# Kernel optimization log

Hardware: AMD Instinct MI355X
Metric: run time of the kernel (lower is better)

Reference implementation:

```python
import jax, jax.numpy as jnp
import numpy as np
from jax import lax

NSAMPLE = 1024
SEM_NUM = 20


def weighted_fps(xyz, w, nsample):
    # xyz: [B,N,3], w: [B,N] -> idx [B,nsample] int32
    # Iterative weighted furthest point sampling: start at index 0, keep the
    # min squared distance to the selected set, pick argmax(min_dist * weight).
    B, N, _ = xyz.shape
    barange = jnp.arange(B)

    def step(carry, _):
        min_d, last = carry                      # [B,N], [B]
        lp = xyz[barange, last]                  # [B,3] last selected points
        d = jnp.sum((xyz - lp[:, None, :]) ** 2, axis=-1)  # [B,N]
        min_d = jnp.minimum(min_d, d)
        nxt = jnp.argmax(min_d * w, axis=1).astype(jnp.int32)
        return (min_d, nxt), nxt

    init = (jnp.full((B, N), 1e10, xyz.dtype), jnp.zeros((B,), jnp.int32))
    _, rest = lax.scan(step, init, None, length=nsample - 1)   # [nsample-1, B]
    idx = jnp.concatenate([jnp.zeros((1, B), jnp.int32), rest], axis=0)
    return idx.T                                               # [B, nsample]


def setup_inputs() -> dict:
    key = jax.random.key(0)
    k1, k2, k3 = jax.random.split(key, 3)
    B, N, C = 16, 16384, 128
    xyz = jax.random.normal(k1, (B, N, 3), dtype=jnp.float32)
    seg_feature = jax.random.normal(k2, (B, C, N), dtype=jnp.float32)
    seg_label = jax.random.randint(k3, (B, N), 0, SEM_NUM, dtype=jnp.int32)
    return {"xyz": xyz, "seg_feature": seg_feature, "seg_label": seg_label}


def reference(xyz, seg_feature, seg_label):
    # class frequency weights: count[b,c] = #points of class c in cloud b
    counts = jnp.sum(jax.nn.one_hot(seg_label, SEM_NUM, dtype=jnp.float32), axis=1)  # [B,SEM]
    seg_weights = jnp.take_along_axis(counts, seg_label, axis=1)                     # [B,N]
    idx = weighted_fps(lax.stop_gradient(xyz), seg_weights, NSAMPLE)                 # [B,S]
    sampled_xyz = jnp.take_along_axis(xyz, idx[:, :, None], axis=1)                  # [B,S,3]
    sample_seg_feature = jnp.take_along_axis(seg_feature, idx[:, None, :], axis=2)   # [B,C,S]
    sample_seg_label = jnp.take_along_axis(seg_label, idx, axis=1)                   # [B,S]
    return sampled_xyz, sample_seg_feature, sample_seg_label
```

## Files before the change

### kernel.cpp

```cpp
#include <hip/hip_runtime.h>


#define FPS_B   16
#define FPS_N   16384
#define FPS_C   128
#define FPS_S   1024
#define FPS_SEM 20
#define FPS_QB  4
#define FPS_MT  1024
#define FPS_MP  4

typedef unsigned long long ull;

__global__ void zero_slots(ull* part) {
  int i = blockIdx.x * blockDim.x + threadIdx.x;
  part[i] = 0ull;
}

__global__ __launch_bounds__(FPS_MT) void wfps_multi(
    const float* __restrict__ xyz,
    const int*   __restrict__ label,
    int*         __restrict__ idx_out,
    ull*         __restrict__ part)
{
  const int b = blockIdx.x & 15;
  const int q = blockIdx.x >> 4;
  const int t = threadIdx.x;

  __shared__ int counts[FPS_SEM];
  __shared__ ull wmax[FPS_S];

  if (t < FPS_SEM) counts[t] = 0;
  wmax[t] = 0ull;
  __syncthreads();

  const int* lab = label + b * FPS_N;
#pragma unroll
  for (int j = 0; j < 16; ++j)
    atomicAdd(&counts[lab[t + j * FPS_MT]], 1);
  __syncthreads();

  const float* xb = xyz + b * FPS_N * 3;
  float px[FPS_MP], py[FPS_MP], pz[FPS_MP], w[FPS_MP], mind[FPS_MP];
#pragma unroll
  for (int k = 0; k < FPS_MP; ++k) {
    int n = q * 4096 + k * 1024 + t;
    px[k] = xb[n * 3 + 0];
    py[k] = xb[n * 3 + 1];
    pz[k] = xb[n * 3 + 2];
    w[k] = (float)counts[lab[n]];
    mind[k] = 1e10f;
    asm("" : "+v"(px[k]), "+v"(py[k]), "+v"(pz[k]), "+v"(w[k]));
  }

  if (q == 0 && t == 0) idx_out[b * FPS_S] = 0;
  float lx = xb[0], ly = xb[1], lz = xb[2];

  ull* pb = part + b * (FPS_QB * FPS_S);

  for (int s = 1; s < FPS_S; ++s) {
    float bs = -1.0f;
    int bk = 0;
#pragma unroll
    for (int k = 0; k < FPS_MP; ++k) {
      float dx = __fsub_rn(px[k], lx);
      float dy = __fsub_rn(py[k], ly);
      float dz = __fsub_rn(pz[k], lz);
      float d  = __fadd_rn(__fadd_rn(__fmul_rn(dx, dx), __fmul_rn(dy, dy)),
                           __fmul_rn(dz, dz));
      float m = fminf(mind[k], d);
      mind[k] = m;
      float sc = __fmul_rn(m, w[k]);
      bool g = sc > bs;
      bs = g ? sc : bs;
      bk = g ? k : bk;
    }
    unsigned n = (unsigned)t + ((unsigned)bk << 10) + ((unsigned)q << 12);
    ull best = ((ull)__float_as_uint(bs) << 32) | (ull)(~n);

#pragma unroll
    for (int off = 32; off > 0; off >>= 1) {
      ull o = __shfl_xor(best, off, 64);
      best = (o > best) ? o : best;
    }
    if ((t & 63) == 0) atomicMax(&wmax[s], best);
    __syncthreads();

    if (t == 0) {
      ull loc = wmax[s];
      __hip_atomic_store(&pb[q * FPS_S + s], loc,
                         __ATOMIC_RELAXED, __HIP_MEMORY_SCOPE_AGENT);
      const int q1 = (q + 1) & 3, q2 = (q + 2) & 3, q3 = (q + 3) & 3;
      ull v1, v2, v3;
      do {
        v1 = __hip_atomic_load(&pb[q1 * FPS_S + s],
                               __ATOMIC_RELAXED, __HIP_MEMORY_SCOPE_AGENT);
        v2 = __hip_atomic_load(&pb[q2 * FPS_S + s],
                               __ATOMIC_RELAXED, __HIP_MEMORY_SCOPE_AGENT);
        v3 = __hip_atomic_load(&pb[q3 * FPS_S + s],
                               __ATOMIC_RELAXED, __HIP_MEMORY_SCOPE_AGENT);
      } while (!(v1 && v2 && v3));
      ull m = loc;
      m = (v1 > m) ? v1 : m;
      m = (v2 > m) ? v2 : m;
      m = (v3 > m) ? v3 : m;
      wmax[s] = m;
    }
    __syncthreads();

    ull g = wmax[s];
    int cur = (int)(~(unsigned)g);
    cur = __builtin_amdgcn_readfirstlane(cur);

    if (q == 0 && t == 0) idx_out[b * FPS_S + s] = cur;

    const float* qq = xb + 3 * cur;
    lx = qq[0]; ly = qq[1]; lz = qq[2];
  }
}

__global__ __launch_bounds__(1024)
__attribute__((amdgpu_waves_per_eu(4, 4)))
void wfps_single(
    const float* __restrict__ xyz,
    const int*   __restrict__ label,
    int*         __restrict__ idx_out)
{
  const int b = blockIdx.x;
  const int t = threadIdx.x;

  __shared__ int counts[FPS_SEM];
  __shared__ ull wmax[FPS_S];

  if (t < FPS_SEM) counts[t] = 0;
  wmax[t] = 0ull;
  __syncthreads();

  const int* lab = label + b * FPS_N;
  int mylab[16];
#pragma unroll
  for (int k = 0; k < 16; ++k) {
    mylab[k] = lab[t + k * 1024];
    atomicAdd(&counts[mylab[k]], 1);
  }
  __syncthreads();

  const float* xb = xyz + b * FPS_N * 3;
  float px[16], py[16], pz[16], w[16], mind[16];
#pragma unroll
  for (int k = 0; k < 16; ++k) {
    int n = t + k * 1024;
    px[k] = xb[n * 3 + 0];
    py[k] = xb[n * 3 + 1];
    pz[k] = xb[n * 3 + 2];
    w[k] = (float)counts[mylab[k]];
    mind[k] = 1e10f;
    asm("" : "+v"(px[k]), "+v"(py[k]), "+v"(pz[k]), "+v"(w[k]));
  }

  if (t == 0) idx_out[b * FPS_S] = 0;
  float lx = xb[0], ly = xb[1], lz = xb[2];

  for (int s = 1; s < FPS_S; ++s) {
    float bs = -1.0f;
    int bk = 0;
#pragma unroll
    for (int k = 0; k < 16; ++k) {
      float dx = __fsub_rn(px[k], lx);
      float dy = __fsub_rn(py[k], ly);
      float dz = __fsub_rn(pz[k], lz);
      float d  = __fadd_rn(__fadd_rn(__fmul_rn(dx, dx), __fmul_rn(dy, dy)),
                           __fmul_rn(dz, dz));
      float m = fminf(mind[k], d);
      mind[k] = m;
      float sc = __fmul_rn(m, w[k]);
      bool g = sc > bs;
      bs = g ? sc : bs;
      bk = g ? k : bk;
    }
    unsigned n = (unsigned)t + ((unsigned)bk << 10);
    ull best = ((ull)__float_as_uint(bs) << 32) | (ull)(~n);
#pragma unroll
    for (int off = 32; off > 0; off >>= 1) {
      ull o = __shfl_xor(best, off, 64);
      best = (o > best) ? o : best;
    }
    if ((t & 63) == 0) atomicMax(&wmax[s], best);
    __syncthreads();
    best = wmax[s];

    int cur = (int)(~(unsigned)best);
    cur = __builtin_amdgcn_readfirstlane(cur);
    if (t == 0) idx_out[b * FPS_S + s] = cur;
    const float* qq = xb + 3 * cur;
    lx = qq[0]; ly = qq[1]; lz = qq[2];
  }
}

__global__ void gather_kernel(
    const float* __restrict__ xyz,
    const float* __restrict__ feat,
    const int*   __restrict__ label,
    const int*   __restrict__ idx,
    float*       __restrict__ out)
{
  const long long FEAT = (long long)FPS_B * FPS_C * FPS_S;
  const int XYZN = FPS_B * FPS_S * 3;
  const int LABN = FPS_B * FPS_S;
  long long i = (long long)blockIdx.x * blockDim.x + threadIdx.x;

  if (i < FEAT) {
    int s = (int)(i & (FPS_S - 1));
    int c = (int)((i >> 10) & (FPS_C - 1));
    int b = (int)(i >> 17);
    int n = idx[b * FPS_S + s];
    out[XYZN + i] = feat[((long long)(b * FPS_C + c)) * FPS_N + n];
  } else if (i < FEAT + XYZN) {
    int j = (int)(i - FEAT);
    int d = j % 3;
    int sb = j / 3;
    int s = sb & (FPS_S - 1);
    int b = sb >> 10;
    int n = idx[b * FPS_S + s];
    out[j] = xyz[((long long)b * FPS_N + n) * 3 + d];
  } else if (i < FEAT + XYZN + LABN) {
    int j = (int)(i - FEAT - XYZN);
    int s = j & (FPS_S - 1);
    int b = j >> 10;
    int n = idx[b * FPS_S + s];
    out[FEAT + XYZN + j] = (float)label[b * FPS_N + n];
  }
}

extern "C" void kernel_launch(void* const* d_in, const int* in_sizes, int n_in,
                              void* d_out, int out_size, void* d_ws, size_t ws_size,
                              hipStream_t stream) {
  const float* xyz   = (const float*)d_in[0];
  const float* feat  = (const float*)d_in[1];
  const int*   label = (const int*)d_in[2];
  float* out = (float*)d_out;
  int*   idx = (int*)d_ws;
  ull*   part = (ull*)((char*)d_ws + 65536);

  const size_t need = 65536 + (size_t)FPS_B * FPS_QB * FPS_S * 8;

  if (ws_size >= need) {
    zero_slots<<<64, 1024, 0, stream>>>(part);
    wfps_multi<<<FPS_B * FPS_QB, FPS_MT, 0, stream>>>(xyz, label, idx, part);
  } else {
    wfps_single<<<FPS_B, 1024, 0, stream>>>(xyz, label, idx);
  }

  const long long total = (long long)FPS_B * FPS_C * FPS_S
                        + (long long)FPS_B * FPS_S * 3
                        + (long long)FPS_B * FPS_S;
  gather_kernel<<<(int)((total + 255) / 256), 256, 0, stream>>>(
      xyz, feat, label, idx, out);
}
```

Before: 1.854 ms.

## Split FPS into 64 single-wave blocks per cloud with sequence-tagged slot exchange

Replaces four 1024-thread blocks per cloud with 64 single-wavefront blocks that each own 256 points. Per-step synchronisation becomes a global double-buffered slot array tagged with the step number and polled by all 64 lanes at once, which removes the __syncthreads and LDS atomic round trips. Class counts move to a separate prep kernel, and the wave reduction uses DPP. The aim is to shorten the latency of each sequential step. In exchange, every step depends on all 64 blocks being co-resident and on cross-CU atomic polling traffic, and the packed key now carries fewer index bits.

```diff
diff --git a/kernel.cpp b/kernel.cpp
--- a/kernel.cpp
+++ b/kernel.cpp
@@ -6,63 +6,85 @@
 #define FPS_C   128
 #define FPS_S   1024
 #define FPS_SEM 20
-#define FPS_QB  4
-#define FPS_MT  1024
-#define FPS_MP  4
+#define FPS_Q   64
+#define FPS_LP  4
 
 typedef unsigned long long ull;
 
-__global__ void zero_slots(ull* part) {
-  int i = blockIdx.x * blockDim.x + threadIdx.x;
-  part[i] = 0ull;
-}
-
-__global__ __launch_bounds__(FPS_MT) void wfps_multi(
+template <int CTRL>
+__device__ __forceinline__ ull dpp_max64(ull v) {
+  unsigned lo = (unsigned)v, hi = (unsigned)(v >> 32);
+  unsigned plo = __builtin_amdgcn_update_dpp(lo, lo, CTRL, 0xF, 0xF, true);
+  unsigned phi = __builtin_amdgcn_update_dpp(hi, hi, CTRL, 0xF, 0xF, true);
+  ull o = ((ull)phi << 32) | plo;
+  return o > v ? o : v;
+}
+
+__device__ __forceinline__ ull wave_max64(ull v) {
+  v = dpp_max64<0xB1>(v);
+  v = dpp_max64<0x4E>(v);
+  v = dpp_max64<0x141>(v);
+  v = dpp_max64<0x140>(v);
+  ull o = __shfl_xor(v, 16, 64); v = (o > v) ? o : v;
+  o = __shfl_xor(v, 32, 64);     v = (o > v) ? o : v;
+  return v;
+}
+
+__global__ __launch_bounds__(1024) void wfps_prep(
+    const int* __restrict__ label,
+    int*       __restrict__ counts,
+    ull*       __restrict__ slots)
+{
+  const int b = blockIdx.x;
+  const int t = threadIdx.x;
+  __shared__ int c[FPS_SEM];
+  if (t < FPS_SEM) c[t] = 0;
+  __syncthreads();
+  const int* lab = label + b * FPS_N;
+#pragma unroll
+  for (int k = 0; k < 16; ++k) atomicAdd(&c[lab[t + k * 1024]], 1);
+  __syncthreads();
+  if (t < FPS_SEM) counts[b * 32 + t] = c[t];
+  if (t < FPS_Q * 2) slots[b * (FPS_Q * 2) + t] = 0ull;
+}
+
+__global__ __launch_bounds__(64) void wfps_fps(
     const float* __restrict__ xyz,
     const int*   __restrict__ label,
+    const int*   __restrict__ counts,
     int*         __restrict__ idx_out,
-    ull*         __restrict__ part)
-{
-  const int b = blockIdx.x & 15;
-  const int q = blockIdx.x >> 4;
-  const int t = threadIdx.x;
-
-  __shared__ int counts[FPS_SEM];
-  __shared__ ull wmax[FPS_S];
-
-  if (t < FPS_SEM) counts[t] = 0;
-  wmax[t] = 0ull;
-  __syncthreads();
-
+    ull*         __restrict__ slots)
+{
+  const int i = blockIdx.x;
+  const int b = (i & 7) + (((i >> 3) & 1) << 3);
+  const int q = i >> 4;
+  const int lane = threadIdx.x;
+
+  const float* xb = xyz + b * FPS_N * 3;
   const int* lab = label + b * FPS_N;
-#pragma unroll
-  for (int j = 0; j < 16; ++j)
-    atomicAdd(&counts[lab[t + j * FPS_MT]], 1);
-  __syncthreads();
-
-  const float* xb = xyz + b * FPS_N * 3;
-  float px[FPS_MP], py[FPS_MP], pz[FPS_MP], w[FPS_MP], mind[FPS_MP];
-#pragma unroll
-  for (int k = 0; k < FPS_MP; ++k) {
-    int n = q * 4096 + k * 1024 + t;
+  const int* cb = counts + b * 32;
+  float px[FPS_LP], py[FPS_LP], pz[FPS_LP], w[FPS_LP], mind[FPS_LP];
+#pragma unroll
+  for (int k = 0; k < FPS_LP; ++k) {
+    int n = (q << 8) + (k << 6) + lane;
     px[k] = xb[n * 3 + 0];
     py[k] = xb[n * 3 + 1];
     pz[k] = xb[n * 3 + 2];
-    w[k] = (float)counts[lab[n]];
+    w[k] = (float)cb[lab[n]];
     mind[k] = 1e10f;
     asm("" : "+v"(px[k]), "+v"(py[k]), "+v"(pz[k]), "+v"(w[k]));
   }
 
-  if (q == 0 && t == 0) idx_out[b * FPS_S] = 0;
+  if (q == 0 && lane == 0) idx_out[(b << 10)] = 0;
   float lx = xb[0], ly = xb[1], lz = xb[2];
 
-  ull* pb = part + b * (FPS_QB * FPS_S);
+  ull* sb = slots + b * (FPS_Q * 2);
 
   for (int s = 1; s < FPS_S; ++s) {
     float bs = -1.0f;
     int bk = 0;
 #pragma unroll
-    for (int k = 0; k < FPS_MP; ++k) {
+    for (int k = 0; k < FPS_LP; ++k) {
       float dx = __fsub_rn(px[k], lx);
       float dy = __fsub_rn(py[k], ly);
       float dz = __fsub_rn(pz[k], lz);
@@ -75,44 +97,26 @@
       bs = g ? sc : bs;
       bk = g ? k : bk;
     }
-    unsigned n = (unsigned)t + ((unsigned)bk << 10) + ((unsigned)q << 12);
-    ull best = ((ull)__float_as_uint(bs) << 32) | (ull)(~n);
-
-#pragma unroll
-    for (int off = 32; off > 0; off >>= 1) {
-      ull o = __shfl_xor(best, off, 64);
-      best = (o > best) ? o : best;
-    }
-    if ((t & 63) == 0) atomicMax(&wmax[s], best);
-    __syncthreads();
-
-    if (t == 0) {
-      ull loc = wmax[s];
-      __hip_atomic_store(&pb[q * FPS_S + s], loc,
+    unsigned n = (unsigned)((q << 8) + (bk << 6) + lane);
+    ull best = ((ull)__float_as_uint(bs) << 32) |
+               (ull)(((unsigned)s << 14) | (16383u - n));
+
+    best = wave_max64(best);
+
+    if (lane == 0)
+      __hip_atomic_store(&sb[(q << 1) + (s & 1)], best,
                          __ATOMIC_RELAXED, __HIP_MEMORY_SCOPE_AGENT);
-      const int q1 = (q + 1) & 3, q2 = (q + 2) & 3, q3 = (q + 3) & 3;
-      ull v1, v2, v3;
-      do {
-        v1 = __hip_atomic_load(&pb[q1 * FPS_S + s],
-                               __ATOMIC_RELAXED, __HIP_MEMORY_SCOPE_AGENT);
-        v2 = __hip_atomic_load(&pb[q2 * FPS_S + s],
-                               __ATOMIC_RELAXED, __HIP_MEMORY_SCOPE_AGENT);
-        v3 = __hip_atomic_load(&pb[q3 * FPS_S + s],
-                               __ATOMIC_RELAXED, __HIP_MEMORY_SCOPE_AGENT);
-      } while (!(v1 && v2 && v3));
-      ull m = loc;
-      m = (v1 > m) ? v1 : m;
-      m = (v2 > m) ? v2 : m;
-      m = (v3 > m) ? v3 : m;
-      wmax[s] = m;
-    }
-    __syncthreads();
-
-    ull g = wmax[s];
-    int cur = (int)(~(unsigned)g);
-    cur = __builtin_amdgcn_readfirstlane(cur);
-
-    if (q == 0 && t == 0) idx_out[b * FPS_S + s] = cur;
+
+    const ull* myslot = &sb[(lane << 1) + (s & 1)];
+    ull v;
+    do {
+      v = __hip_atomic_load(myslot, __ATOMIC_RELAXED, __HIP_MEMORY_SCOPE_AGENT);
+    } while (__ballot((unsigned)((v >> 14) & 0x3FF) == (unsigned)s) != ~0ull);
+
+    ull g = wave_max64(v);
+    int cur = 16383 - (int)(g & 0x3FFF);
+
+    if (q == 0 && lane == 0) idx_out[(b << 10) + s] = cur;
 
     const float* qq = xb + 3 * cur;
     lx = qq[0]; ly = qq[1]; lz = qq[2];
@@ -128,14 +132,11 @@
 {
   const int b = blockIdx.x;
   const int t = threadIdx.x;
-
   __shared__ int counts[FPS_SEM];
   __shared__ ull wmax[FPS_S];
-
   if (t < FPS_SEM) counts[t] = 0;
   wmax[t] = 0ull;
   __syncthreads();
-
   const int* lab = label + b * FPS_N;
   int mylab[16];
 #pragma unroll
@@ -144,7 +145,6 @@
     atomicAdd(&counts[mylab[k]], 1);
   }
   __syncthreads();
-
   const float* xb = xyz + b * FPS_N * 3;
   float px[16], py[16], pz[16], w[16], mind[16];
 #pragma unroll
@@ -157,10 +157,8 @@
     mind[k] = 1e10f;
     asm("" : "+v"(px[k]), "+v"(py[k]), "+v"(pz[k]), "+v"(w[k]));
   }
-
   if (t == 0) idx_out[b * FPS_S] = 0;
   float lx = xb[0], ly = xb[1], lz = xb[2];
-
   for (int s = 1; s < FPS_S; ++s) {
     float bs = -1.0f;
     int bk = 0;
@@ -188,9 +186,7 @@
     if ((t & 63) == 0) atomicMax(&wmax[s], best);
     __syncthreads();
     best = wmax[s];
-
     int cur = (int)(~(unsigned)best);
-    cur = __builtin_amdgcn_readfirstlane(cur);
     if (t == 0) idx_out[b * FPS_S + s] = cur;
     const float* qq = xb + 3 * cur;
     lx = qq[0]; ly = qq[1]; lz = qq[2];
@@ -239,14 +235,16 @@
   const float* feat  = (const float*)d_in[1];
   const int*   label = (const int*)d_in[2];
   float* out = (float*)d_out;
-  int*   idx = (int*)d_ws;
-  ull*   part = (ull*)((char*)d_ws + 65536);
-
-  const size_t need = 65536 + (size_t)FPS_B * FPS_QB * FPS_S * 8;
+
+  int* idx    = (int*)d_ws;
+  int* counts = (int*)((char*)d_ws + 65536);
+  ull* slots  = (ull*)((char*)d_ws + 67584);
+
+  const size_t need = 65536 + 2048 + (size_t)FPS_B * FPS_Q * 2 * 8;
 
   if (ws_size >= need) {
-    zero_slots<<<64, 1024, 0, stream>>>(part);
-    wfps_multi<<<FPS_B * FPS_QB, FPS_MT, 0, stream>>>(xyz, label, idx, part);
+    wfps_prep<<<FPS_B, 1024, 0, stream>>>(label, counts, slots);
+    wfps_fps<<<FPS_B * FPS_Q, 64, 0, stream>>>(xyz, label, counts, idx, slots);
   } else {
     wfps_single<<<FPS_B, 1024, 0, stream>>>(xyz, label, idx);
   }
```

After: 4.464 ms. +140.8%, slower.
